# Optimization experiments

Measured on AMD Instinct MI355X. Metric: run time of the kernel, lower is better.

## Reference

```python
import jax, jax.numpy as jnp
import numpy as np


def setup_inputs() -> dict:
    key = jax.random.key(0)
    k1, k2, k3, k4 = jax.random.split(key, 4)
    batch, n_channels, t = 4, 2048, 2048
    n_blocks, block_size, ks = 128, 64, 16
    n_block_row = n_channels // block_size  # 32
    x = jax.random.normal(k1, (batch, n_channels, t), dtype=jnp.float32)
    block_values = jax.random.normal(k2, (n_blocks, block_size, block_size, ks), dtype=jnp.float32) * 0.05
    cols = jax.random.randint(k3, (n_blocks,), 0, n_block_row, dtype=jnp.int32)
    rows = jax.random.randint(k4, (n_blocks,), 0, n_block_row, dtype=jnp.int32)
    return {"x": x, "block_values": block_values, "cols": cols, "rows": rows}


def reference(x, block_values, cols, rows):
    # x: (B, C, T); block_values: (n_blocks, bs, bs, ks)
    batch, n_channels, t = x.shape
    n_blocks, bs, _, ks = block_values.shape
    n_block_row = -(-n_channels // bs)
    pad = n_block_row * bs - n_channels
    if pad > 0:
        x = jnp.pad(x, ((0, 0), (0, pad), (0, 0)))
    xb = x.reshape(batch, n_block_row, bs, t)
    # gather active block rows: (B, n_blocks, bs, T) -> (B, n_blocks*bs, T)
    x_unfold = xb[:, cols].reshape(batch, n_blocks * bs, t)
    # grouped causal conv: weights shared across batch, groups = n_blocks
    W = block_values.reshape(n_blocks * bs, bs, ks)  # (O, I/g, K)
    o = jax.lax.conv_general_dilated(
        x_unfold, W,
        window_strides=(1,),
        padding=[(ks - 1, 0)],  # causal: equals padding=ks-1 then [..., :t]
        dimension_numbers=("NCH", "OIH", "NCH"),
        feature_group_count=n_blocks,
    )  # (B, n_blocks*bs, T)
    o = o.reshape(batch, n_blocks, bs, t)
    # scatter-add block outputs into their target block rows
    y = jnp.zeros((batch, n_block_row, bs, t), o.dtype).at[:, rows].add(o)
    y = y.reshape(batch, n_block_row * bs, t)
    return y[:, :n_channels, :]
```

## Files before the change

kernel.cpp:

```cpp
#include <hip/hip_runtime.h>
#include <hip/hip_bf16.h>
#include <stdint.h>

typedef __bf16 bf16_t;
typedef bf16_t bf16x8 __attribute__((ext_vector_type(8)));
typedef float f32x4 __attribute__((ext_vector_type(4)));

#define T_LEN 2048
#define C_LEN 2048
#define NB 128
#define TN 256
#define SROWS 2064
#define XROWS 288

#define GLL(gp, lp) __builtin_amdgcn_global_load_lds( \
    (const __attribute__((address_space(1))) uint32_t*)(gp), \
    (__attribute__((address_space(3))) uint32_t*)(lp), 16, 0, 0)

__global__ __launch_bounds__(256) void prepack_kernel(
    const float* __restrict__ bv, bf16_t* __restrict__ wpk)
{
  const int blk = blockIdx.x;
  const int mt  = blockIdx.y;
  const int tid = threadIdx.x;
  __shared__ float lw[16 * 64 * 17];

  const float* src = bv + (size_t)blk * 65536 + (size_t)mt * 16384;
  for (int p = 0; p < 16; ++p) {
    int idx = p * 1024 + tid * 4;
    const float4 v = *(const float4*)(src + idx);
    int o = idx >> 10;
    int i = (idx >> 4) & 63;
    int k = idx & 15;
    float* d = &lw[(o * 64 + i) * 17 + k];
    d[0] = v.x; d[1] = v.y; d[2] = v.z; d[3] = v.w;
  }
  __syncthreads();

  const int e0 = tid * 2;
  const int l  = e0 >> 3;
  const int j  = e0 & 7;
  const int o  = l & 15;
  for (int ks = 0; ks < 32; ++ks) {
    const int k  = ks >> 1;
    const int i0 = (ks & 1) * 32 + (l >> 4) * 8 + j;
    const float a = lw[(o * 64 + i0) * 17 + k];
    const float b = lw[(o * 64 + i0 + 1) * 17 + k];
    const uint16_t ba = __builtin_bit_cast(uint16_t, (bf16_t)a);
    const uint16_t bb = __builtin_bit_cast(uint16_t, (bf16_t)b);
    const uint32_t packed = (uint32_t)ba | ((uint32_t)bb << 16);
    const size_t off = ((((size_t)blk * 32 + ks) * 4 + mt) * 512) + e0;
    *(uint32_t*)(wpk + off) = packed;
  }
}

__global__ __launch_bounds__(256) void padzero_kernel(bf16_t* __restrict__ S)
{
  const int p = blockIdx.x;
  const size_t g = (p < 64) ? ((size_t)(p >> 4) * SROWS + (p & 15))
                            : ((size_t)4 * SROWS + (p - 64));
  uint4 z = {0u, 0u, 0u, 0u};
  *(uint4*)(S + g * C_LEN + (size_t)threadIdx.x * 8) = z;
}

__global__ __launch_bounds__(256) void xprep_kernel(
    const float* __restrict__ x, bf16_t* __restrict__ S)
{
  const int tb = blockIdx.x, cb = blockIdx.y, n = blockIdx.z;
  const int tid = threadIdx.x;
  __shared__ float lt[64 * 67 + 4];

  #pragma unroll
  for (int p = 0; p < 4; ++p) {
    const int idx = p * 256 + tid;
    const int c   = idx >> 4;
    const int t4  = (idx & 15) * 4;
    const float4 v = *(const float4*)(
        x + ((size_t)n * C_LEN + cb * 64 + c) * T_LEN + tb * 64 + t4);
    float* d = &lt[c * 67 + t4];
    d[0] = v.x; d[1] = v.y; d[2] = v.z; d[3] = v.w;
  }
  __syncthreads();

  #pragma unroll
  for (int p = 0; p < 2; ++p) {
    const int idx = p * 256 + tid;
    const int tl  = idx >> 3;
    const int seg = idx & 7;
    const int t   = tb * 64 + tl;
    const int cbase = (seg * 8) ^ ((t & 7) << 3);
    uint32_t w[4];
    #pragma unroll
    for (int h = 0; h < 4; ++h) {
      const float a = lt[(cbase + 2 * h) * 67 + tl];
      const float b = lt[(cbase + 2 * h + 1) * 67 + tl];
      const uint16_t ba = __builtin_bit_cast(uint16_t, (bf16_t)a);
      const uint16_t bb = __builtin_bit_cast(uint16_t, (bf16_t)b);
      w[h] = (uint32_t)ba | ((uint32_t)bb << 16);
    }
    uint4 u4 = {w[0], w[1], w[2], w[3]};
    *(uint4*)(S + ((size_t)n * SROWS + 16 + t) * C_LEN + cb * 64 + seg * 8) = u4;
  }
}

__global__ __launch_bounds__(256, 2) void bsconv_kernel(
    const bf16_t* __restrict__ S, const bf16_t* __restrict__ wpk,
    const int* __restrict__ cols, const int* __restrict__ rows,
    float* __restrict__ y)
{
  const int tt = blockIdx.x, tr = blockIdx.y, n = blockIdx.z;
  const int t0 = tt * TN;
  const int tid = threadIdx.x;
  const int lane = tid & 63, wv = tid >> 6;

  __shared__ __attribute__((aligned(16))) bf16_t xst[XROWS * 64];
  __shared__ __attribute__((aligned(16))) bf16_t wlds[2][8192];
  __shared__ int rlds[NB], clds[NB];

  if (tid < NB) rlds[tid] = rows[tid];
  else          clds[tid - NB] = cols[tid - NB];
  __syncthreads();

  f32x4 acc[4][4];
  #pragma unroll
  for (int a = 0; a < 4; ++a)
    #pragma unroll
    for (int b = 0; b < 4; ++b) {
      f32x4 z = {0.f, 0.f, 0.f, 0.f};
      acc[a][b] = z;
    }

  const size_t srow0 = (size_t)n * SROWS + t0;
  const int lxb = wv * 1024 + lane * 16;

  for (int blk = 0; blk < NB; ++blk) {
    if (rlds[blk] != tr) continue;
    const int cb = clds[blk];
    const bf16_t* wblk = wpk + (size_t)blk * 65536;

    #pragma unroll
    for (int q = 0; q < 9; ++q) {
      const int lb = q * 4096 + lxb;
      const int u  = lb >> 7;
      const int ib = (lb >> 1) & 63;
      const bf16_t* gp = S + (srow0 + u) * C_LEN + cb * 64 + ib;
      GLL(gp, (char*)xst + lb);
    }
    #pragma unroll
    for (int p = 0; p < 4; ++p) {
      const int lb = p * 4096 + lxb;
      GLL(wblk + (lb >> 1), (char*)wlds[0] + lb);
    }

    for (int ch = 0; ch < 8; ++ch) {
      if (ch < 7) {
        bf16_t* wd = wlds[(ch + 1) & 1];
        const bf16_t* gsrc = wblk + (size_t)(ch + 1) * 8192;
        #pragma unroll
        for (int p = 0; p < 4; ++p) {
          const int lb = p * 4096 + lxb;
          GLL(gsrc + (lb >> 1), (char*)wd + lb);
        }
        asm volatile("s_waitcnt vmcnt(4)" ::: "memory");
      } else {
        asm volatile("s_waitcnt vmcnt(0)" ::: "memory");
      }
      __builtin_amdgcn_s_barrier();
      __builtin_amdgcn_sched_barrier(0);

      const bf16_t* wl = wlds[ch & 1];
      #pragma unroll
      for (int ksl = 0; ksl < 4; ++ksl) {
        const int ks = ch * 4 + ksl;
        const int k  = ks >> 1;
        const int ih = (ks & 1) * 32;
        bf16x8 afr[4];
        #pragma unroll
        for (int mt = 0; mt < 4; ++mt)
          afr[mt] = *(const bf16x8*)(wl + ((ksl * 4 + mt) * 64 + lane) * 8);
        const int ub = wv * 64 + (lane & 15) + k + 1;
        const int scol = (ih + ((lane >> 4) & 3) * 8) ^ ((ub & 7) << 3);
        bf16x8 bfr[4];
        #pragma unroll
        for (int nt = 0; nt < 4; ++nt)
          bfr[nt] = *(const bf16x8*)(xst + (ub + nt * 16) * 64 + scol);
        #pragma unroll
        for (int mt = 0; mt < 4; ++mt)
          #pragma unroll
          for (int nt = 0; nt < 4; ++nt)
            acc[mt][nt] = __builtin_amdgcn_mfma_f32_16x16x32_bf16(
                afr[mt], bfr[nt], acc[mt][nt], 0, 0, 0);
      }
      __builtin_amdgcn_sched_barrier(0);
      __builtin_amdgcn_s_barrier();
    }
  }

  const int mlo = ((lane >> 4) & 3) * 4, nn = lane & 15;
  #pragma unroll
  for (int mt = 0; mt < 4; ++mt) {
    #pragma unroll
    for (int nt = 0; nt < 4; ++nt) {
      const int t = t0 + wv * 64 + nt * 16 + nn;
      float* yp = y + ((size_t)n * C_LEN + (size_t)(tr * 64 + mt * 16 + mlo)) * T_LEN + t;
      #pragma unroll
      for (int r = 0; r < 4; ++r)
        yp[(size_t)r * T_LEN] = acc[mt][nt][r];
    }
  }
}

extern "C" void kernel_launch(void* const* d_in, const int* in_sizes, int n_in,
                              void* d_out, int out_size, void* d_ws, size_t ws_size,
                              hipStream_t stream) {
  const float* x   = (const float*)d_in[0];
  const float* bv  = (const float*)d_in[1];
  const int* cols  = (const int*)d_in[2];
  const int* rows  = (const int*)d_in[3];
  float* y = (float*)d_out;

  bf16_t* wpk = (bf16_t*)d_ws;
  bf16_t* S   = (bf16_t*)((char*)d_ws + 16777216);

  prepack_kernel<<<dim3(128, 4), dim3(256), 0, stream>>>(bv, wpk);
  padzero_kernel<<<dim3(80), dim3(256), 0, stream>>>(S);
  xprep_kernel<<<dim3(32, 32, 4), dim3(256), 0, stream>>>(x, S);
  bsconv_kernel<<<dim3(8, 32, 4), dim3(256), 0, stream>>>(S, wpk, cols, rows, y);
}
```

Baseline: 194.1 us.

## Compact active blocks via ballot, double-buffer x tiles, read weights from global

Builds a compact list of the blocks that target this row tile, using wave ballots and popcount, instead of scanning all 128 entries. It double-buffers the x tile in LDS so the next block's gather is issued while the current block is computed. Weights are now read straight from global memory rather than staged through LDS chunks. This removes the per-chunk barriers and the weight LDS traffic, but exposes global-load latency in the MFMA inner loop and repeats the same weight reads across the four waves.

New measurement: 265.4 us. +36.8%, slower.

```diff
diff --git a/kernel.cpp b/kernel.cpp
--- a/kernel.cpp
+++ b/kernel.cpp
@@ -113,13 +113,26 @@
   const int tid = threadIdx.x;
   const int lane = tid & 63, wv = tid >> 6;
 
-  __shared__ __attribute__((aligned(16))) bf16_t xst[XROWS * 64];
-  __shared__ __attribute__((aligned(16))) bf16_t wlds[2][8192];
-  __shared__ int rlds[NB], clds[NB];
-
-  if (tid < NB) rlds[tid] = rows[tid];
-  else          clds[tid - NB] = cols[tid - NB];
-  __syncthreads();
+  __shared__ __attribute__((aligned(16))) bf16_t xst[2][XROWS * 64];
+  __shared__ int alist[NB];
+  __shared__ int clds[NB];
+  __shared__ unsigned long long wmask[2];
+
+  {
+    const int r = (tid < NB) ? rows[tid] : -1;
+    if (tid < NB) clds[tid] = cols[tid];
+    const bool match = (r == tr);
+    const unsigned long long m = __ballot(match);
+    if (wv < 2 && lane == 0) wmask[wv] = m;
+    __syncthreads();
+    if (match) {
+      int pos = __popcll(wmask[wv] & ((1ull << lane) - 1ull));
+      if (wv == 1) pos += __popcll(wmask[0]);
+      alist[pos] = tid;
+    }
+    __syncthreads();
+  }
+  const int cnt = __popcll(wmask[0]) + __popcll(wmask[1]);
 
   f32x4 acc[4][4];
   #pragma unroll
@@ -133,66 +146,45 @@
   const size_t srow0 = (size_t)n * SROWS + t0;
   const int lxb = wv * 1024 + lane * 16;
 
-  for (int blk = 0; blk < NB; ++blk) {
-    if (rlds[blk] != tr) continue;
-    const int cb = clds[blk];
-    const bf16_t* wblk = wpk + (size_t)blk * 65536;
-
+  auto issue_x = [&](int cb, int buf) {
     #pragma unroll
     for (int q = 0; q < 9; ++q) {
       const int lb = q * 4096 + lxb;
       const int u  = lb >> 7;
       const int ib = (lb >> 1) & 63;
-      const bf16_t* gp = S + (srow0 + u) * C_LEN + cb * 64 + ib;
-      GLL(gp, (char*)xst + lb);
-    }
-    #pragma unroll
-    for (int p = 0; p < 4; ++p) {
-      const int lb = p * 4096 + lxb;
-      GLL(wblk + (lb >> 1), (char*)wlds[0] + lb);
-    }
-
-    for (int ch = 0; ch < 8; ++ch) {
-      if (ch < 7) {
-        bf16_t* wd = wlds[(ch + 1) & 1];
-        const bf16_t* gsrc = wblk + (size_t)(ch + 1) * 8192;
-        #pragma unroll
-        for (int p = 0; p < 4; ++p) {
-          const int lb = p * 4096 + lxb;
-          GLL(gsrc + (lb >> 1), (char*)wd + lb);
-        }
-        asm volatile("s_waitcnt vmcnt(4)" ::: "memory");
-      } else {
-        asm volatile("s_waitcnt vmcnt(0)" ::: "memory");
-      }
-      __builtin_amdgcn_s_barrier();
-      __builtin_amdgcn_sched_barrier(0);
-
-      const bf16_t* wl = wlds[ch & 1];
-      #pragma unroll
-      for (int ksl = 0; ksl < 4; ++ksl) {
-        const int ks = ch * 4 + ksl;
-        const int k  = ks >> 1;
-        const int ih = (ks & 1) * 32;
-        bf16x8 afr[4];
-        #pragma unroll
-        for (int mt = 0; mt < 4; ++mt)
-          afr[mt] = *(const bf16x8*)(wl + ((ksl * 4 + mt) * 64 + lane) * 8);
-        const int ub = wv * 64 + (lane & 15) + k + 1;
-        const int scol = (ih + ((lane >> 4) & 3) * 8) ^ ((ub & 7) << 3);
-        bf16x8 bfr[4];
+      GLL(S + (srow0 + u) * C_LEN + cb * 64 + ib, (char*)xst[buf] + lb);
+    }
+  };
+
+  if (cnt > 0) issue_x(clds[alist[0]], 0);
+
+  for (int j = 0; j < cnt; ++j) {
+    __syncthreads();
+    if (j + 1 < cnt) issue_x(clds[alist[j + 1]], (j + 1) & 1);
+
+    const bf16_t* __restrict__ wb = wpk + (size_t)alist[j] * 65536;
+    const bf16_t* xb = xst[j & 1];
+
+    #pragma unroll 4
+    for (int ks = 0; ks < 32; ++ks) {
+      const int k  = ks >> 1;
+      const int ih = (ks & 1) * 32;
+      bf16x8 afr[4];
+      #pragma unroll
+      for (int mt = 0; mt < 4; ++mt)
+        afr[mt] = *(const bf16x8*)(wb + (size_t)((ks * 4 + mt) * 64 + lane) * 8);
+      const int ub   = wv * 64 + (lane & 15) + k + 1;
+      const int scol = (ih + ((lane >> 4) & 3) * 8) ^ ((ub & 7) << 3);
+      bf16x8 bfr[4];
+      #pragma unroll
+      for (int nt = 0; nt < 4; ++nt)
+        bfr[nt] = *(const bf16x8*)(xb + (ub + nt * 16) * 64 + scol);
+      #pragma unroll
+      for (int mt = 0; mt < 4; ++mt)
         #pragma unroll
         for (int nt = 0; nt < 4; ++nt)
-          bfr[nt] = *(const bf16x8*)(xst + (ub + nt * 16) * 64 + scol);
-        #pragma unroll
-        for (int mt = 0; mt < 4; ++mt)
-          #pragma unroll
-          for (int nt = 0; nt < 4; ++nt)
-            acc[mt][nt] = __builtin_amdgcn_mfma_f32_16x16x32_bf16(
-                afr[mt], bfr[nt], acc[mt][nt], 0, 0, 0);
-      }
-      __builtin_amdgcn_sched_barrier(0);
-      __builtin_amdgcn_s_barrier();
+          acc[mt][nt] = __builtin_amdgcn_mfma_f32_16x16x32_bf16(
+              afr[mt], bfr[nt], acc[mt][nt], 0, 0, 0);
     }
   }
 
```
